# Optimization experiments

Measured on AMD Instinct MI355X. Metric: run time of the kernel, lower is better.

The kernel has to match this reference:

```python
import jax, jax.numpy as jnp
import numpy as np

B, N, D, H, DFF = 8, 1024, 1024, 16, 4096
HD = D // H

def _xavier(key, shape):
    fan_in, fan_out = shape[1], shape[0]
    limit = float(np.sqrt(6.0 / (fan_in + fan_out)))
    return jax.random.uniform(key, shape, jnp.float32, -limit, limit)

def setup_inputs() -> dict:
    key = jax.random.key(0)
    ks = jax.random.split(key, 8)
    return {
        'src':    jax.random.normal(ks[0], (B, N, D), jnp.float32),
        'wqkv':   _xavier(ks[1], (3 * D, D)),
        'bqkv':   jnp.zeros((3 * D,), jnp.float32),
        'wo':     _xavier(ks[2], (D, D)),
        'bo':     jnp.zeros((D,), jnp.float32),
        'g1':     jnp.ones((D,), jnp.float32),
        'b1':     jnp.zeros((D,), jnp.float32),
        'g2':     jnp.ones((D,), jnp.float32),
        'b2':     jnp.zeros((D,), jnp.float32),
        'w_gate': _xavier(ks[3], (DFF, D)),
        'b_gate': jnp.zeros((DFF,), jnp.float32),
        'w_up':   _xavier(ks[4], (DFF, D)),
        'b_up':   jnp.zeros((DFF,), jnp.float32),
        'w_down': _xavier(ks[5], (D, DFF)),
        'b_down': jnp.zeros((D,), jnp.float32),
    }

def _layernorm(x, g, b, eps=1e-5):
    mu = jnp.mean(x, axis=-1, keepdims=True)
    var = jnp.var(x, axis=-1, keepdims=True)
    return (x - mu) * jax.lax.rsqrt(var + eps) * g + b

def _alibi_slopes(heads):
    # m_h = 2^(-8h/H), h = 1..H
    return jnp.asarray(2.0 ** (-8.0 * np.arange(1, heads + 1) / heads), jnp.float32)

def _attention(x, wqkv, bqkv, wo, bo):
    qkv = x @ wqkv.T + bqkv                      # [B,N,3D]
    q, k, v = jnp.split(qkv, 3, axis=-1)
    def heads(t):
        return t.reshape(B, N, H, HD).transpose(0, 2, 1, 3)  # [B,H,N,D]
    q, k, v = heads(q), heads(k), heads(v)
    # ALiBi bias: -slope * |i - j|, broadcast over batch
    pos = jnp.arange(N, dtype=jnp.float32)
    dist = jnp.abs(pos[:, None] - pos[None, :])  # [N,N]
    bias = -_alibi_slopes(H)[:, None, None] * dist  # [H,N,N]
    scale = 1.0 / np.sqrt(HD)
    scores = jnp.einsum('bhnd,bhmd->bhnm', q, k) * scale + bias[None]
    attn = jax.nn.softmax(scores, axis=-1)
    out = jnp.einsum('bhnm,bhmd->bhnd', attn, v)
    out = out.transpose(0, 2, 1, 3).reshape(B, N, D)
    return out @ wo.T + bo

def _swiglu(x, w_gate, b_gate, w_up, b_up, w_down, b_down):
    gate = jax.nn.silu(x @ w_gate.T + b_gate)
    up = x @ w_up.T + b_up
    return (gate * up) @ w_down.T + b_down

def reference(src, wqkv, bqkv, wo, bo, g1, b1, g2, b2,
              w_gate, b_gate, w_up, b_up, w_down, b_down):
    x = src + _attention(_layernorm(src, g1, b1), wqkv, bqkv, wo, bo)
    x = x + _swiglu(_layernorm(x, g2, b2), w_gate, b_gate, w_up, b_up, w_down, b_down)
    return x
```

## Files before the change

### kernel.cpp

```cpp
#include <hip/hip_runtime.h>

#define Bz 8
#define Nz 1024
#define Dz 1024
#define Hz 16
#define HDz 64
#define DFFz 4096

typedef __attribute__((ext_vector_type(8))) __bf16 bh8;
typedef __attribute__((ext_vector_type(4))) __bf16 bh4;
typedef __attribute__((ext_vector_type(4))) float f4;

#define GLOAD16(gp, lp) __builtin_amdgcn_global_load_lds( \
    (__attribute__((address_space(1))) void*)(gp), \
    (__attribute__((address_space(3))) void*)(lp), 16, 0, 0)

__global__ __launch_bounds__(256) void cvt_k(const float* __restrict__ in,
                                             __bf16* __restrict__ out, int n4) {
    int i = blockIdx.x * 256 + threadIdx.x;
    if (i < n4) {
        float4 v = ((const float4*)in)[i];
        bh4 o;
        o[0] = (__bf16)v.x; o[1] = (__bf16)v.y; o[2] = (__bf16)v.z; o[3] = (__bf16)v.w;
        ((bh4*)out)[i] = o;
    }
}

__global__ __launch_bounds__(256) void ln_k(const float* __restrict__ x,
                                            const float* __restrict__ g,
                                            const float* __restrict__ bb,
                                            __bf16* __restrict__ out) {
    const int row = blockIdx.x, t = threadIdx.x;
    const float4 v = ((const float4*)(x + (size_t)row * Dz))[t];
    float s = v.x + v.y + v.z + v.w;
    float s2 = v.x * v.x + v.y * v.y + v.z * v.z + v.w * v.w;
#pragma unroll
    for (int off = 32; off > 0; off >>= 1) {
        s += __shfl_down(s, off);
        s2 += __shfl_down(s2, off);
    }
    __shared__ float ps[4], ps2[4];
    if ((t & 63) == 0) { ps[t >> 6] = s; ps2[t >> 6] = s2; }
    __syncthreads();
    float ts = 0.f, ts2 = 0.f;
#pragma unroll
    for (int i = 0; i < 4; i++) { ts += ps[i]; ts2 += ps2[i]; }
    const float mean = ts * (1.f / Dz);
    const float var = ts2 * (1.f / Dz) - mean * mean;
    const float inv = rsqrtf(var + 1e-5f);
    const float4 gv = ((const float4*)g)[t];
    const float4 bv = ((const float4*)bb)[t];
    bh4 o;
    o[0] = (__bf16)((v.x - mean) * inv * gv.x + bv.x);
    o[1] = (__bf16)((v.y - mean) * inv * gv.y + bv.y);
    o[2] = (__bf16)((v.z - mean) * inv * gv.z + bv.z);
    o[3] = (__bf16)((v.w - mean) * inv * gv.w + bv.w);
    *(bh4*)&out[(size_t)row * Dz + t * 4] = o;
}

template <int EPI>
__global__ __launch_bounds__(256) void gemm128(
    const __bf16* __restrict__ A, const __bf16* __restrict__ W,
    const float* __restrict__ bias, void* __restrict__ outp,
    const float* __restrict__ addf, const __bf16* __restrict__ upb,
    int M, int N, int K) {
    __shared__ __align__(16) __bf16 lsA[128 * 32];
    __shared__ __align__(16) __bf16 lsB[128 * 32];
    const int t = threadIdx.x;
    const int w = t >> 6, l = t & 63;
    const int brow = blockIdx.y, bcol = blockIdx.x;

    const __bf16* Ag = A + (size_t)(brow * 128 + (t >> 2)) * K + (t & 3) * 8;
    const __bf16* Wg = W + (size_t)(bcol * 128 + (t >> 2)) * K + (t & 3) * 8;
    __bf16* lA0 = lsA + w * 512;
    __bf16* lB0 = lsB + w * 512;

    const f4 zf = {0.f, 0.f, 0.f, 0.f};
    f4 acc[4][4];
#pragma unroll
    for (int m = 0; m < 4; m++)
#pragma unroll
        for (int n = 0; n < 4; n++) acc[m][n] = zf;

    const int lo = l & 15, hi = l >> 4;
    const int rowA = (w >> 1) * 64 + lo;
    const int colB = (w & 1) * 64 + lo;
    const int kk = hi * 8;

    for (int k0 = 0; k0 < K; k0 += 32) {
        GLOAD16(Ag + k0, lA0);
        GLOAD16(Ag + (size_t)64 * K + k0, lA0 + 64 * 32);
        GLOAD16(Wg + k0, lB0);
        GLOAD16(Wg + (size_t)64 * K + k0, lB0 + 64 * 32);
        __syncthreads();
        bh8 af[4], bfv[4];
#pragma unroll
        for (int m = 0; m < 4; m++) af[m] = *(const bh8*)&lsA[(rowA + m * 16) * 32 + kk];
#pragma unroll
        for (int n = 0; n < 4; n++) bfv[n] = *(const bh8*)&lsB[(colB + n * 16) * 32 + kk];
#pragma unroll
        for (int m = 0; m < 4; m++)
#pragma unroll
            for (int n = 0; n < 4; n++)
                acc[m][n] = __builtin_amdgcn_mfma_f32_16x16x32_bf16(af[m], bfv[n], acc[m][n], 0, 0, 0);
        __syncthreads();
    }

    const int gr0 = brow * 128 + (w >> 1) * 64;
    const int gc0 = bcol * 128 + (w & 1) * 64;
#pragma unroll
    for (int m = 0; m < 4; m++)
#pragma unroll
        for (int n = 0; n < 4; n++) {
            const int col = gc0 + n * 16 + lo;
            const float bv = bias[col];
#pragma unroll
            for (int j = 0; j < 4; j++) {
                const int row = gr0 + m * 16 + hi * 4 + j;
                const size_t idx = (size_t)row * N + col;
                const float v = acc[m][n][j] + bv;
                if (EPI == 0) {
                    ((__bf16*)outp)[idx] = (__bf16)v;
                } else if (EPI == 1 || EPI == 2) {
                    ((float*)outp)[idx] = addf[idx] + v;
                } else {
                    const float u = (float)upb[idx];
                    const float sv = v / (1.f + __expf(-v));
                    ((__bf16*)outp)[idx] = (__bf16)(sv * u);
                }
            }
        }
}

__global__ __launch_bounds__(256) void attn_k(const __bf16* __restrict__ qkv,
                                              __bf16* __restrict__ out) {
    const int t = threadIdx.x, w = t >> 6, l = t & 63;
    const int qt = blockIdx.x, h = blockIdx.y, b = blockIdx.z;
    const int qbase = qt * 64;
    const int lo = l & 15, hi = l >> 4;
    const float slope = exp2f(-0.5f * (float)(h + 1));

    const size_t base = (size_t)b * Nz * 3072 + h * 64;
    const __bf16* qp = qkv + base;
    const __bf16* kp = qkv + base + 1024;
    const __bf16* vp = qkv + base + 2048;

    __shared__ __align__(16) __bf16 lsK[64 * 72];
    __shared__ __align__(16) __bf16 lsVt[64 * 72];
    __shared__ __align__(16) __bf16 lsP[4 * 16 * 72];

    const int myq = qbase + w * 16 + lo;
    const bh8 qf0 = *(const bh8*)(qp + (size_t)myq * 3072 + hi * 8);
    const bh8 qf1 = *(const bh8*)(qp + (size_t)myq * 3072 + 32 + hi * 8);

    const f4 zf = {0.f, 0.f, 0.f, 0.f};
    float m_run[4], l_run[4];
    f4 oacc[4];
#pragma unroll
    for (int jj = 0; jj < 4; jj++) { m_run[jj] = -1e30f; l_run[jj] = 0.f; }
#pragma unroll
    for (int n = 0; n < 4; n++) oacc[n] = zf;

    for (int j0 = 0; j0 < Nz; j0 += 64) {
        __syncthreads();
        {
            const int jr = t >> 2, d0 = (t & 3) * 16;
            const __bf16* krow = kp + (size_t)(j0 + jr) * 3072 + d0;
            *(bh8*)&lsK[jr * 72 + d0] = *(const bh8*)krow;
            *(bh8*)&lsK[jr * 72 + d0 + 8] = *(const bh8*)(krow + 8);
        }
        {
            const int d = t & 63;
            bh8 t0, t1;
#pragma unroll
            for (int jj = 0; jj < 8; jj++) t0[jj] = vp[(size_t)(j0 + w * 16 + jj) * 3072 + d];
#pragma unroll
            for (int jj = 0; jj < 8; jj++) t1[jj] = vp[(size_t)(j0 + w * 16 + 8 + jj) * 3072 + d];
            *(bh8*)&lsVt[d * 72 + w * 16] = t0;
            *(bh8*)&lsVt[d * 72 + w * 16 + 8] = t1;
        }
        __syncthreads();

        float vals[4][4];
#pragma unroll
        for (int c = 0; c < 4; c++) {
            const bh8 kf0 = *(const bh8*)&lsK[(c * 16 + lo) * 72 + hi * 8];
            const bh8 kf1 = *(const bh8*)&lsK[(c * 16 + lo) * 72 + 32 + hi * 8];
            f4 s = zf;
            s = __builtin_amdgcn_mfma_f32_16x16x32_bf16(qf0, kf0, s, 0, 0, 0);
            s = __builtin_amdgcn_mfma_f32_16x16x32_bf16(qf1, kf1, s, 0, 0, 0);
            const int gj = j0 + c * 16 + lo;
#pragma unroll
            for (int jj = 0; jj < 4; jj++) {
                const int gq = qbase + w * 16 + hi * 4 + jj;
                vals[c][jj] = s[jj] * 0.125f - slope * fabsf((float)(gq - gj));
            }
        }
        float mc[4];
#pragma unroll
        for (int jj = 0; jj < 4; jj++)
            mc[jj] = fmaxf(fmaxf(vals[0][jj], vals[1][jj]), fmaxf(vals[2][jj], vals[3][jj]));
#pragma unroll
        for (int off = 8; off > 0; off >>= 1)
#pragma unroll
            for (int jj = 0; jj < 4; jj++) mc[jj] = fmaxf(mc[jj], __shfl_xor(mc[jj], off));
        float corr[4], psum[4];
#pragma unroll
        for (int jj = 0; jj < 4; jj++) {
            const float mn = fmaxf(m_run[jj], mc[jj]);
            corr[jj] = __expf(m_run[jj] - mn);
            m_run[jj] = mn;
            psum[jj] = 0.f;
        }
#pragma unroll
        for (int c = 0; c < 4; c++)
#pragma unroll
            for (int jj = 0; jj < 4; jj++) {
                const float p = __expf(vals[c][jj] - m_run[jj]);
                vals[c][jj] = p;
                psum[jj] += p;
            }
#pragma unroll
        for (int off = 8; off > 0; off >>= 1)
#pragma unroll
            for (int jj = 0; jj < 4; jj++) psum[jj] += __shfl_xor(psum[jj], off);
#pragma unroll
        for (int jj = 0; jj < 4; jj++) l_run[jj] = l_run[jj] * corr[jj] + psum[jj];
#pragma unroll
        for (int n = 0; n < 4; n++)
#pragma unroll
            for (int jj = 0; jj < 4; jj++) oacc[n][jj] *= corr[jj];

#pragma unroll
        for (int c = 0; c < 4; c++)
#pragma unroll
            for (int jj = 0; jj < 4; jj++)
                lsP[(w * 16 + hi * 4 + jj) * 72 + c * 16 + lo] = (__bf16)vals[c][jj];

        const bh8 pa0 = *(const bh8*)&lsP[(w * 16 + lo) * 72 + hi * 8];
        const bh8 pa1 = *(const bh8*)&lsP[(w * 16 + lo) * 72 + 32 + hi * 8];
#pragma unroll
        for (int n = 0; n < 4; n++) {
            const bh8 vf0 = *(const bh8*)&lsVt[(n * 16 + lo) * 72 + hi * 8];
            const bh8 vf1 = *(const bh8*)&lsVt[(n * 16 + lo) * 72 + 32 + hi * 8];
            oacc[n] = __builtin_amdgcn_mfma_f32_16x16x32_bf16(pa0, vf0, oacc[n], 0, 0, 0);
            oacc[n] = __builtin_amdgcn_mfma_f32_16x16x32_bf16(pa1, vf1, oacc[n], 0, 0, 0);
        }
    }

#pragma unroll
    for (int n = 0; n < 4; n++)
#pragma unroll
        for (int jj = 0; jj < 4; jj++) {
            const int gq = qbase + w * 16 + hi * 4 + jj;
            const int d = n * 16 + lo;
            out[((size_t)b * Nz + gq) * Dz + h * 64 + d] = (__bf16)(oacc[n][jj] / l_run[jj]);
        }
}

extern "C" void kernel_launch(void* const* d_in, const int* in_sizes, int n_in,
                              void* d_out, int out_size, void* d_ws, size_t ws_size,
                              hipStream_t stream) {
    const float* src  = (const float*)d_in[0];
    const float* wqkv = (const float*)d_in[1];
    const float* bqkv = (const float*)d_in[2];
    const float* wo   = (const float*)d_in[3];
    const float* bo   = (const float*)d_in[4];
    const float* g1   = (const float*)d_in[5];
    const float* b1   = (const float*)d_in[6];
    const float* g2   = (const float*)d_in[7];
    const float* b2   = (const float*)d_in[8];
    const float* wg   = (const float*)d_in[9];
    const float* bg   = (const float*)d_in[10];
    const float* wu   = (const float*)d_in[11];
    const float* bu   = (const float*)d_in[12];
    const float* wd   = (const float*)d_in[13];
    const float* bd   = (const float*)d_in[14];
    float* out = (float*)d_out;

    __bf16* wqkv_b = (__bf16*)d_ws;
    __bf16* wo_b   = wqkv_b + (size_t)3072 * 1024;
    __bf16* wg_b   = wo_b + (size_t)1024 * 1024;
    __bf16* wu_b   = wg_b + (size_t)4096 * 1024;
    __bf16* wd_b   = wu_b + (size_t)4096 * 1024;
    __bf16* lnbuf  = wd_b + (size_t)1024 * 4096;
    __bf16* qkv    = lnbuf + (size_t)8192 * 1024;
    __bf16* attno  = qkv + (size_t)8192 * 3072;
    float*  x1     = (float*)(attno + (size_t)8192 * 1024);
    __bf16* hb     = qkv;

    cvt_k<<<3072, 256, 0, stream>>>(wqkv, wqkv_b, 3072 * 1024 / 4);
    cvt_k<<<1024, 256, 0, stream>>>(wo, wo_b, 1024 * 1024 / 4);
    cvt_k<<<4096, 256, 0, stream>>>(wg, wg_b, 4096 * 1024 / 4);
    cvt_k<<<4096, 256, 0, stream>>>(wu, wu_b, 4096 * 1024 / 4);
    cvt_k<<<4096, 256, 0, stream>>>(wd, wd_b, 1024 * 4096 / 4);

    ln_k<<<8192, 256, 0, stream>>>(src, g1, b1, lnbuf);
    gemm128<0><<<dim3(3072 / 128, 8192 / 128), 256, 0, stream>>>(
        lnbuf, wqkv_b, bqkv, qkv, nullptr, nullptr, 8192, 3072, 1024);
    attn_k<<<dim3(16, 16, 8), 256, 0, stream>>>(qkv, attno);
    gemm128<1><<<dim3(1024 / 128, 8192 / 128), 256, 0, stream>>>(
        attno, wo_b, bo, x1, src, nullptr, 8192, 1024, 1024);

    ln_k<<<8192, 256, 0, stream>>>(x1, g2, b2, lnbuf);
    gemm128<0><<<dim3(4096 / 128, 8192 / 128), 256, 0, stream>>>(
        lnbuf, wu_b, bu, hb, nullptr, nullptr, 8192, 4096, 1024);
    gemm128<3><<<dim3(4096 / 128, 8192 / 128), 256, 0, stream>>>(
        lnbuf, wg_b, bg, hb, nullptr, hb, 8192, 4096, 1024);
    gemm128<2><<<dim3(1024 / 128, 8192 / 128), 256, 0, stream>>>(
        hb, wd_b, bd, out, x1, nullptr, 8192, 1024, 4096);
}
```

Baseline: 755.8 us.

## Double-buffer GEMM LDS tiles and swizzle attention K/P shared layouts

The GEMM main loop now uses two LDS buffers so the global-to-LDS load of the next K tile is issued before the MFMA work on the current tile, with a single barrier per iteration. The aim is to overlap memory latency with compute. In the attention kernel, the padded K and P shared arrays are replaced by unpadded 64-wide rows with an XOR swizzle, to avoid bank conflicts and save LDS. The cost is double the GEMM LDS footprint, which could reduce occupancy.

Result: faster. 726.7 us (-3.8%).

```diff
diff --git a/kernel.cpp b/kernel.cpp
--- a/kernel.cpp
+++ b/kernel.cpp
@@ -64,16 +64,14 @@
     const float* __restrict__ bias, void* __restrict__ outp,
     const float* __restrict__ addf, const __bf16* __restrict__ upb,
     int M, int N, int K) {
-    __shared__ __align__(16) __bf16 lsA[128 * 32];
-    __shared__ __align__(16) __bf16 lsB[128 * 32];
+    __shared__ __align__(16) __bf16 lsA[2 * 128 * 32];
+    __shared__ __align__(16) __bf16 lsB[2 * 128 * 32];
     const int t = threadIdx.x;
     const int w = t >> 6, l = t & 63;
     const int brow = blockIdx.y, bcol = blockIdx.x;
 
     const __bf16* Ag = A + (size_t)(brow * 128 + (t >> 2)) * K + (t & 3) * 8;
     const __bf16* Wg = W + (size_t)(bcol * 128 + (t >> 2)) * K + (t & 3) * 8;
-    __bf16* lA0 = lsA + w * 512;
-    __bf16* lB0 = lsB + w * 512;
 
     const f4 zf = {0.f, 0.f, 0.f, 0.f};
     f4 acc[4][4];
@@ -87,24 +85,41 @@
     const int colB = (w & 1) * 64 + lo;
     const int kk = hi * 8;
 
-    for (int k0 = 0; k0 < K; k0 += 32) {
-        GLOAD16(Ag + k0, lA0);
-        GLOAD16(Ag + (size_t)64 * K + k0, lA0 + 64 * 32);
-        GLOAD16(Wg + k0, lB0);
-        GLOAD16(Wg + (size_t)64 * K + k0, lB0 + 64 * 32);
+#define STAGE(P, KOFF) do { \
+        GLOAD16(Ag + (KOFF), lsA + (P) * 4096 + w * 512); \
+        GLOAD16(Ag + (size_t)64 * K + (KOFF), lsA + (P) * 4096 + w * 512 + 64 * 32); \
+        GLOAD16(Wg + (KOFF), lsB + (P) * 4096 + w * 512); \
+        GLOAD16(Wg + (size_t)64 * K + (KOFF), lsB + (P) * 4096 + w * 512 + 64 * 32); \
+    } while (0)
+
+#define COMPUTE(P) do { \
+        const __bf16* la = lsA + (P) * 4096; \
+        const __bf16* lb = lsB + (P) * 4096; \
+        bh8 af[4], bfv[4]; \
+        _Pragma("unroll") \
+        for (int m = 0; m < 4; m++) af[m] = *(const bh8*)&la[(rowA + m * 16) * 32 + kk]; \
+        _Pragma("unroll") \
+        for (int n = 0; n < 4; n++) bfv[n] = *(const bh8*)&lb[(colB + n * 16) * 32 + kk]; \
+        _Pragma("unroll") \
+        for (int m = 0; m < 4; m++) \
+            _Pragma("unroll") \
+            for (int n = 0; n < 4; n++) \
+                acc[m][n] = __builtin_amdgcn_mfma_f32_16x16x32_bf16(af[m], bfv[n], acc[m][n], 0, 0, 0); \
+    } while (0)
+
+    const int nt = K >> 5;
+    int cur = 0;
+    STAGE(0, 0);
+    __syncthreads();
+    for (int kt = 0; kt < nt - 1; ++kt) {
+        STAGE(cur ^ 1, (kt + 1) * 32);
+        COMPUTE(cur);
         __syncthreads();
-        bh8 af[4], bfv[4];
-#pragma unroll
-        for (int m = 0; m < 4; m++) af[m] = *(const bh8*)&lsA[(rowA + m * 16) * 32 + kk];
-#pragma unroll
-        for (int n = 0; n < 4; n++) bfv[n] = *(const bh8*)&lsB[(colB + n * 16) * 32 + kk];
-#pragma unroll
-        for (int m = 0; m < 4; m++)
-#pragma unroll
-            for (int n = 0; n < 4; n++)
-                acc[m][n] = __builtin_amdgcn_mfma_f32_16x16x32_bf16(af[m], bfv[n], acc[m][n], 0, 0, 0);
-        __syncthreads();
+        cur ^= 1;
     }
+    COMPUTE(cur);
+#undef STAGE
+#undef COMPUTE
 
     const int gr0 = brow * 128 + (w >> 1) * 64;
     const int gc0 = bcol * 128 + (w & 1) * 64;
@@ -145,9 +160,9 @@
     const __bf16* kp = qkv + base + 1024;
     const __bf16* vp = qkv + base + 2048;
 
-    __shared__ __align__(16) __bf16 lsK[64 * 72];
+    __shared__ __align__(16) __bf16 lsK[64 * 64];
     __shared__ __align__(16) __bf16 lsVt[64 * 72];
-    __shared__ __align__(16) __bf16 lsP[4 * 16 * 72];
+    __shared__ __align__(16) __bf16 lsP[4 * 16 * 64];
 
     const int myq = qbase + w * 16 + lo;
     const bh8 qf0 = *(const bh8*)(qp + (size_t)myq * 3072 + hi * 8);
@@ -161,13 +176,15 @@
 #pragma unroll
     for (int n = 0; n < 4; n++) oacc[n] = zf;
 
+    const int jr = t >> 2, d0 = (t & 3) * 16;
+
     for (int j0 = 0; j0 < Nz; j0 += 64) {
         __syncthreads();
         {
-            const int jr = t >> 2, d0 = (t & 3) * 16;
             const __bf16* krow = kp + (size_t)(j0 + jr) * 3072 + d0;
-            *(bh8*)&lsK[jr * 72 + d0] = *(const bh8*)krow;
-            *(bh8*)&lsK[jr * 72 + d0 + 8] = *(const bh8*)(krow + 8);
+            const int sw = (jr & 7) * 8;
+            *(bh8*)&lsK[jr * 64 + (d0 ^ sw)] = *(const bh8*)krow;
+            *(bh8*)&lsK[jr * 64 + ((d0 + 8) ^ sw)] = *(const bh8*)(krow + 8);
         }
         {
             const int d = t & 63;
@@ -184,8 +201,10 @@
         float vals[4][4];
 #pragma unroll
         for (int c = 0; c < 4; c++) {
-            const bh8 kf0 = *(const bh8*)&lsK[(c * 16 + lo) * 72 + hi * 8];
-            const bh8 kf1 = *(const bh8*)&lsK[(c * 16 + lo) * 72 + 32 + hi * 8];
+            const int krw = c * 16 + lo;
+            const int swr = (krw & 7);
+            const bh8 kf0 = *(const bh8*)&lsK[krw * 64 + 8 * (hi ^ swr)];
+            const bh8 kf1 = *(const bh8*)&lsK[krw * 64 + 8 * ((4 + hi) ^ swr)];
             f4 s = zf;
             s = __builtin_amdgcn_mfma_f32_16x16x32_bf16(qf0, kf0, s, 0, 0, 0);
             s = __builtin_amdgcn_mfma_f32_16x16x32_bf16(qf1, kf1, s, 0, 0, 0);
@@ -234,11 +253,15 @@
 #pragma unroll
         for (int c = 0; c < 4; c++)
 #pragma unroll
-            for (int jj = 0; jj < 4; jj++)
-                lsP[(w * 16 + hi * 4 + jj) * 72 + c * 16 + lo] = (__bf16)vals[c][jj];
-
-        const bh8 pa0 = *(const bh8*)&lsP[(w * 16 + lo) * 72 + hi * 8];
-        const bh8 pa1 = *(const bh8*)&lsP[(w * 16 + lo) * 72 + 32 + hi * 8];
+            for (int jj = 0; jj < 4; jj++) {
+                const int q = hi * 4 + jj;
+                lsP[w * 1024 + q * 64 + ((c * 16 + lo) ^ ((q & 7) * 8))] = (__bf16)vals[c][jj];
+            }
+
+        const int psw = (lo & 7);
+        const bh8 pa0 = *(const bh8*)&lsP[w * 1024 + lo * 64 + 8 * (hi ^ psw)];
+        const bh8 pa1 = *(const bh8*)&lsP[w * 1024 + lo * 64 + 8 * ((4 + hi) ^ psw)];
+
 #pragma unroll
         for (int n = 0; n < 4; n++) {
             const bh8 vf0 = *(const bh8*)&lsVt[(n * 16 + lo) * 72 + hi * 8];
```
